# Optimization experiments

Hardware: AMD Instinct MI355X
Metric: run time of the kernel (lower is better)

Reference implementation:

```python
import jax, jax.numpy as jnp
import numpy as np

STRIDE = 1
PADDING = 1
GROUPS = 1


def setup_inputs() -> dict:
    key = jax.random.key(0)
    kx, kw, kb = jax.random.split(key, 3)
    x_int = jax.random.randint(kx, (16, 256, 56, 56), 0, 127, dtype=jnp.int32)
    weight_int = jax.random.randint(kw, (256, 256, 3, 3), 0, 127, dtype=jnp.int32)
    bias_int = jax.random.randint(kb, (256,), 0, 127, dtype=jnp.int32)
    return {"x_int": x_int, "weight_int": weight_int, "bias_int": bias_int}


def reference(x_int, weight_int, bias_int):
    # Integer conv2d with int32 accumulation, exactly F.conv2d semantics.
    y = jax.lax.conv_general_dilated(
        x_int,
        weight_int,
        window_strides=(STRIDE, STRIDE),
        padding=((PADDING, PADDING), (PADDING, PADDING)),
        dimension_numbers=("NCHW", "OIHW", "NCHW"),
        feature_group_count=GROUPS,
    )
    # bias broadcast over [B, Cout, H, W]
    return y + bias_int[None, :, None, None]
```

## Files before the change

### kernel.cpp

```cpp
#include <hip/hip_runtime.h>


typedef int v4i __attribute__((ext_vector_type(4)));

#define X8_ROWSTRIDE 3712
#define X8_IMGSTRIDE (58 * X8_ROWSTRIDE)
#define X8_BYTES (64 * X8_IMGSTRIDE)
#define W8_TILE 36864
#define XS_OFF 36864
#define LDS_BYTES 59648

typedef const __attribute__((address_space(1))) unsigned char* gptr_t;
typedef __attribute__((address_space(3))) unsigned char* lptr_t;

__global__ __launch_bounds__(256)
void pack_all(const int* __restrict__ x, const int* __restrict__ wgt,
              unsigned char* __restrict__ ws8) {
  const int blk = blockIdx.x;
  if (blk < 3712) {
    const int row = blk % 58;
    const int cb  = blk / 58;
    const int chunk = cb >> 4, b = cb & 15;
    const int tid = threadIdx.x;
    if (tid >= 232) return;
    const int slot = tid >> 2, p = tid & 3;
    union { v4i v; unsigned char c[16]; } u;
    u.v = (v4i){0, 0, 0, 0};
    if (row >= 1 && row <= 56 && slot >= 1 && slot <= 56) {
      const int q = (p - (slot >> 2)) & 3;
      const unsigned char* src = (const unsigned char*)(x
          + ((b * 256 + chunk * 64 + q * 16) * 56 + (row - 1)) * 56 + (slot - 1));
      #pragma unroll
      for (int j = 0; j < 16; ++j) u.c[j] = src[j * 12544];
    }
    *(v4i*)(ws8 + cb * X8_IMGSTRIDE + row * X8_ROWSTRIDE + slot * 64 + p * 16) = u.v;
  } else {
    const int g  = (blk - 3712) * 256 + threadIdx.x;
    const int p  = g & 3;
    const int sp = g >> 2;
    const int s  = sp % 9;
    const int ct = sp / 9;
    const int co64 = ct & 63;
    const int tcch = ct >> 6;
    const int tc = tcch >> 2, chunk = tcch & 3;
    const int q = (p - ((co64 >> 2) & 3)) & 3;
    const unsigned char* src = (const unsigned char*)(wgt
        + (tc * 64 + co64) * 2304 + (chunk * 64 + q * 16) * 9 + s);
    union { v4i v; unsigned char c[16]; } u;
    #pragma unroll
    for (int j = 0; j < 16; ++j) u.c[j] = src[j * 36];
    *(v4i*)(ws8 + X8_BYTES + ct * 576 + s * 64 + p * 16) = u.v;
  }
}

__global__ __launch_bounds__(512, 4)
void conv_main(const unsigned char* __restrict__ ws8, const int* __restrict__ bias,
               int* __restrict__ out) {
  __shared__ __align__(16) unsigned char lds[LDS_BYTES];
  unsigned char* wls = lds;
  unsigned char* xs  = lds + XS_OFF;
  const unsigned char* x8 = ws8;
  const unsigned char* w8 = ws8 + X8_BYTES;

  const int tid = threadIdx.x, lane = tid & 63, wv = tid >> 6;
  const int q = lane >> 4, m = lane & 15;
  const int cw = wv & 1;
  const int pw = wv >> 1;
  const int tc = blockIdx.x;
  const int h0 = blockIdx.y * 4;
  const int b  = blockIdx.z;

  const unsigned char* arow = wls + (cw * 32 + m) * 576 + ((q + (m >> 2)) & 3) * 16;
  int boff[3][4];
  #pragma unroll
  for (int kw = 0; kw < 3; ++kw)
    #pragma unroll
    for (int nt = 0; nt < 4; ++nt) {
      int slot = nt * 16 + m + kw;
      slot = slot > 57 ? 57 : slot;
      boff[kw][nt] = slot * 64 + ((q + (slot >> 2)) & 3) * 16;
    }

  v4i acc[2][4];
  #pragma unroll
  for (int i = 0; i < 2; ++i)
    #pragma unroll
    for (int j = 0; j < 4; ++j) acc[i][j] = (v4i){0, 0, 0, 0};

  for (int c = 0; c < 4; ++c) {
    __syncthreads();
    const unsigned char* wg = w8 + (tc * 4 + c) * W8_TILE;
    #pragma unroll
    for (int i = 0; i < 5; ++i) {
      const int j = i * 8 + wv;
      if (j < 36)
        __builtin_amdgcn_global_load_lds((gptr_t)(wg + j * 1024 + lane * 16),
                                         (lptr_t)(wls + j * 1024), 16, 0, 0);
    }
    const unsigned char* xg = x8 + (c * 16 + b) * X8_IMGSTRIDE + h0 * X8_ROWSTRIDE;
    #pragma unroll
    for (int i = 0; i < 3; ++i) {
      const int j = i * 8 + wv;
      if (j < 22)
        __builtin_amdgcn_global_load_lds((gptr_t)(xg + j * 1024 + lane * 16),
                                         (lptr_t)(xs + j * 1024), 16, 0, 0);
    }
    __syncthreads();
    #pragma unroll
    for (int kh = 0; kh < 3; ++kh) {
      const unsigned char* xr = xs + (pw + kh) * X8_ROWSTRIDE;
      #pragma unroll
      for (int kw = 0; kw < 3; ++kw) {
        const int s = kh * 3 + kw;
        const v4i a0 = *(const v4i*)(arow + s * 64);
        const v4i a1 = *(const v4i*)(arow + 16 * 576 + s * 64);
        #pragma unroll
        for (int nt = 0; nt < 4; ++nt) {
          const v4i bf = *(const v4i*)(xr + boff[kw][nt]);
          acc[0][nt] = __builtin_amdgcn_mfma_i32_16x16x64_i8(a0, bf, acc[0][nt], 0, 0, 0);
          acc[1][nt] = __builtin_amdgcn_mfma_i32_16x16x64_i8(a1, bf, acc[1][nt], 0, 0, 0);
        }
      }
    }
  }

  const int h = h0 + pw;
  #pragma unroll
  for (int half = 0; half < 2; ++half) {
    #pragma unroll
    for (int nt = 0; nt < 4; ++nt) {
      const int wp = nt * 16 + m;
      if (wp < 56) {
        #pragma unroll
        for (int r = 0; r < 4; ++r) {
          const int co = tc * 64 + cw * 32 + half * 16 + q * 4 + r;
          out[((b * 256 + co) * 56 + h) * 56 + wp] = acc[half][nt][r] + bias[co];
        }
      }
    }
  }
}

extern "C" void kernel_launch(void* const* d_in, const int* in_sizes, int n_in,
                              void* d_out, int out_size, void* d_ws, size_t ws_size,
                              hipStream_t stream) {
  const int* x    = (const int*)d_in[0];
  const int* w    = (const int*)d_in[1];
  const int* bias = (const int*)d_in[2];
  unsigned char* ws8 = (unsigned char*)d_ws;
  hipLaunchKernelGGL(pack_all, dim3(3712 + 144), dim3(256), 0, stream, x, w, ws8);
  hipLaunchKernelGGL(conv_main, dim3(4, 14, 16), dim3(512), 0, stream,
                     ws8, bias, (int*)d_out);
}
```

Baseline: 136.2 us.

## Switch conv to 32x32x32 int8 MFMA with 32-channel chunks and 128-thread blocks

Result: no change. 135.9 us (-0.2%).

```diff
diff --git a/kernel.cpp b/kernel.cpp
--- a/kernel.cpp
+++ b/kernel.cpp
@@ -1,141 +1,141 @@
 #include <hip/hip_runtime.h>
 
 
-typedef int v4i __attribute__((ext_vector_type(4)));
+typedef int v4i  __attribute__((ext_vector_type(4)));
+typedef int v16i __attribute__((ext_vector_type(16)));
 
-#define X8_ROWSTRIDE 3712
-#define X8_IMGSTRIDE (58 * X8_ROWSTRIDE)
-#define X8_BYTES (64 * X8_IMGSTRIDE)
-#define W8_TILE 36864
-#define XS_OFF 36864
-#define LDS_BYTES 59648
+#define X8_ROWSTRIDE 1856
+#define X8_IMGSTRIDE 107648
+#define X8_BYTES     13778944
+#define W8_CHUNK     18432
 
 typedef const __attribute__((address_space(1))) unsigned char* gptr_t;
 typedef __attribute__((address_space(3))) unsigned char* lptr_t;
 
+__device__ __forceinline__ int pack4(const int* p, int stride) {
+  return (p[0] & 255) | ((p[stride] & 255) << 8) |
+         ((p[2 * stride] & 255) << 16) | ((p[3 * stride] & 255) << 24);
+}
+
 __global__ __launch_bounds__(256)
 void pack_all(const int* __restrict__ x, const int* __restrict__ wgt,
               unsigned char* __restrict__ ws8) {
-  const int blk = blockIdx.x;
-  if (blk < 3712) {
-    const int row = blk % 58;
-    const int cb  = blk / 58;
-    const int chunk = cb >> 4, b = cb & 15;
-    const int tid = threadIdx.x;
-    if (tid >= 232) return;
-    const int slot = tid >> 2, p = tid & 3;
-    union { v4i v; unsigned char c[16]; } u;
-    u.v = (v4i){0, 0, 0, 0};
+  const int g = blockIdx.x * 256 + threadIdx.x;
+  if (g < 861184) {
+    const int p = g & 1;
+    int t = g >> 1;
+    const int slot = t % 58; t /= 58;
+    const int row  = t % 58;
+    const int cb   = t / 58;
+    v4i v = (v4i){0, 0, 0, 0};
     if (row >= 1 && row <= 56 && slot >= 1 && slot <= 56) {
-      const int q = (p - (slot >> 2)) & 3;
-      const unsigned char* src = (const unsigned char*)(x
-          + ((b * 256 + chunk * 64 + q * 16) * 56 + (row - 1)) * 56 + (slot - 1));
-      #pragma unroll
-      for (int j = 0; j < 16; ++j) u.c[j] = src[j * 12544];
+      const int chunk = cb >> 4, b = cb & 15;
+      const int srcg = (p + slot) & 1;
+      const int ci0 = chunk * 32 + srcg * 16;
+      const int* src = x + (b * 256 + ci0) * 3136 + (row - 1) * 56 + (slot - 1);
+      v = (v4i){pack4(src, 3136), pack4(src + 4 * 3136, 3136),
+                pack4(src + 8 * 3136, 3136), pack4(src + 12 * 3136, 3136)};
     }
-    *(v4i*)(ws8 + cb * X8_IMGSTRIDE + row * X8_ROWSTRIDE + slot * 64 + p * 16) = u.v;
+    *(v4i*)(ws8 + (cb * 58 + row) * X8_ROWSTRIDE + slot * 32 + p * 16) = v;
   } else {
-    const int g  = (blk - 3712) * 256 + threadIdx.x;
-    const int p  = g & 3;
-    const int sp = g >> 2;
-    const int s  = sp % 9;
-    const int ct = sp / 9;
-    const int co64 = ct & 63;
-    const int tcch = ct >> 6;
-    const int tc = tcch >> 2, chunk = tcch & 3;
-    const int q = (p - ((co64 >> 2) & 3)) & 3;
-    const unsigned char* src = (const unsigned char*)(wgt
-        + (tc * 64 + co64) * 2304 + (chunk * 64 + q * 16) * 9 + s);
-    union { v4i v; unsigned char c[16]; } u;
-    #pragma unroll
-    for (int j = 0; j < 16; ++j) u.c[j] = src[j * 36];
-    *(v4i*)(ws8 + X8_BYTES + ct * 576 + s * 64 + p * 16) = u.v;
+    const int gw = g - 861184;
+    const int p = gw & 1;
+    int t = gw >> 1;
+    const int tap = t % 9;  t /= 9;
+    const int co = t & 63;
+    const int tcc = t >> 6;
+    const int chunk = tcc & 7, cotile = tcc >> 3;
+    const int srcg = (p + co) & 1;
+    const int ci0 = chunk * 32 + srcg * 16;
+    const int* src = wgt + ((cotile * 64 + co) * 256 + ci0) * 9 + tap;
+    v4i v = (v4i){pack4(src, 9), pack4(src + 36, 9),
+                  pack4(src + 72, 9), pack4(src + 108, 9)};
+    *(v4i*)(ws8 + X8_BYTES + (t * 9 + tap) * 32 + p * 16) = v;
   }
 }
 
-__global__ __launch_bounds__(512, 4)
+__global__ __launch_bounds__(128, 2)
 void conv_main(const unsigned char* __restrict__ ws8, const int* __restrict__ bias,
                int* __restrict__ out) {
-  __shared__ __align__(16) unsigned char lds[LDS_BYTES];
+  __shared__ __align__(16) unsigned char lds[18432 + 12288];
+  __shared__ int bls[64];
   unsigned char* wls = lds;
-  unsigned char* xs  = lds + XS_OFF;
-  const unsigned char* x8 = ws8;
-  const unsigned char* w8 = ws8 + X8_BYTES;
+  unsigned char* xs  = lds + 18432;
 
   const int tid = threadIdx.x, lane = tid & 63, wv = tid >> 6;
-  const int q = lane >> 4, m = lane & 15;
-  const int cw = wv & 1;
-  const int pw = wv >> 1;
+  const int n = lane & 31, gq = lane >> 5;
   const int tc = blockIdx.x;
   const int h0 = blockIdx.y * 4;
   const int b  = blockIdx.z;
 
-  const unsigned char* arow = wls + (cw * 32 + m) * 576 + ((q + (m >> 2)) & 3) * 16;
+  if (tid < 64) bls[tid] = bias[tc * 64 + tid];
+
+  const int abase = n * 288 + (((gq + n) & 1) << 4);
   int boff[3][4];
   #pragma unroll
   for (int kw = 0; kw < 3; ++kw)
     #pragma unroll
-    for (int nt = 0; nt < 4; ++nt) {
-      int slot = nt * 16 + m + kw;
-      slot = slot > 57 ? 57 : slot;
-      boff[kw][nt] = slot * 64 + ((q + (slot >> 2)) & 3) * 16;
+    for (int bt = 0; bt < 4; ++bt) {
+      int slot = bt * 16 + (n & 15) + kw;
+      if (slot > 57) slot = 57;
+      boff[kw][bt] = slot * 32 + (((gq + slot) & 1) << 4);
     }
+  const int rbase = (2 * wv + (n >> 4)) * X8_ROWSTRIDE;
 
-  v4i acc[2][4];
+  v16i acc[2][4];
   #pragma unroll
   for (int i = 0; i < 2; ++i)
     #pragma unroll
-    for (int j = 0; j < 4; ++j) acc[i][j] = (v4i){0, 0, 0, 0};
+    for (int j = 0; j < 4; ++j)
+      acc[i][j] = (v16i){0,0,0,0,0,0,0,0,0,0,0,0,0,0,0,0};
 
-  for (int c = 0; c < 4; ++c) {
+  const unsigned char* wg = ws8 + X8_BYTES + tc * (8 * W8_CHUNK);
+  const unsigned char* xg = ws8 + b * X8_IMGSTRIDE + h0 * X8_ROWSTRIDE;
+
+  for (int c = 0; c < 8; ++c) {
     __syncthreads();
-    const unsigned char* wg = w8 + (tc * 4 + c) * W8_TILE;
+    const gptr_t wsrc = (gptr_t)(wg + c * W8_CHUNK);
     #pragma unroll
-    for (int i = 0; i < 5; ++i) {
-      const int j = i * 8 + wv;
-      if (j < 36)
-        __builtin_amdgcn_global_load_lds((gptr_t)(wg + j * 1024 + lane * 16),
-                                         (lptr_t)(wls + j * 1024), 16, 0, 0);
-    }
-    const unsigned char* xg = x8 + (c * 16 + b) * X8_IMGSTRIDE + h0 * X8_ROWSTRIDE;
+    for (int i = 0; i < 9; ++i)
+      __builtin_amdgcn_global_load_lds(wsrc + i * 2048 + tid * 16,
+                                       (lptr_t)(wls + i * 2048 + tid * 16), 16, 0, 0);
+    const gptr_t xsrc = (gptr_t)(xg + c * (16 * X8_IMGSTRIDE));
     #pragma unroll
-    for (int i = 0; i < 3; ++i) {
-      const int j = i * 8 + wv;
-      if (j < 22)
-        __builtin_amdgcn_global_load_lds((gptr_t)(xg + j * 1024 + lane * 16),
-                                         (lptr_t)(xs + j * 1024), 16, 0, 0);
-    }
+    for (int i = 0; i < 6; ++i)
+      __builtin_amdgcn_global_load_lds(xsrc + i * 2048 + tid * 16,
+                                       (lptr_t)(xs + i * 2048 + tid * 16), 16, 0, 0);
     __syncthreads();
     #pragma unroll
     for (int kh = 0; kh < 3; ++kh) {
-      const unsigned char* xr = xs + (pw + kh) * X8_ROWSTRIDE;
+      const unsigned char* xr = xs + rbase + kh * X8_ROWSTRIDE;
       #pragma unroll
       for (int kw = 0; kw < 3; ++kw) {
-        const int s = kh * 3 + kw;
-        const v4i a0 = *(const v4i*)(arow + s * 64);
-        const v4i a1 = *(const v4i*)(arow + 16 * 576 + s * 64);
+        const int tap = kh * 3 + kw;
+        const v4i a0 = *(const v4i*)(wls + abase + tap * 32);
+        const v4i a1 = *(const v4i*)(wls + 9216 + abase + tap * 32);
         #pragma unroll
-        for (int nt = 0; nt < 4; ++nt) {
-          const v4i bf = *(const v4i*)(xr + boff[kw][nt]);
-          acc[0][nt] = __builtin_amdgcn_mfma_i32_16x16x64_i8(a0, bf, acc[0][nt], 0, 0, 0);
-          acc[1][nt] = __builtin_amdgcn_mfma_i32_16x16x64_i8(a1, bf, acc[1][nt], 0, 0, 0);
+        for (int bt = 0; bt < 4; ++bt) {
+          const v4i bb = *(const v4i*)(xr + boff[kw][bt]);
+          acc[0][bt] = __builtin_amdgcn_mfma_i32_32x32x32_i8(a0, bb, acc[0][bt], 0, 0, 0);
+          acc[1][bt] = __builtin_amdgcn_mfma_i32_32x32x32_i8(a1, bb, acc[1][bt], 0, 0, 0);
         }
       }
     }
   }
 
-  const int h = h0 + pw;
+  const int h = h0 + 2 * wv + (n >> 4);
+  const int wbase = lane & 15;
   #pragma unroll
-  for (int half = 0; half < 2; ++half) {
+  for (int ct = 0; ct < 2; ++ct) {
     #pragma unroll
-    for (int nt = 0; nt < 4; ++nt) {
-      const int wp = nt * 16 + m;
-      if (wp < 56) {
-        #pragma unroll
-        for (int r = 0; r < 4; ++r) {
-          const int co = tc * 64 + cw * 32 + half * 16 + q * 4 + r;
-          out[((b * 256 + co) * 56 + h) * 56 + wp] = acc[half][nt][r] + bias[co];
-        }
+    for (int r = 0; r < 16; ++r) {
+      const int co64 = ct * 32 + (r & 3) + 8 * (r >> 2) + 4 * gq;
+      const int bv = bls[co64];
+      int* orow = out + ((b * 256 + tc * 64 + co64) * 56 + h) * 56;
+      #pragma unroll
+      for (int bt = 0; bt < 4; ++bt) {
+        const int w0 = bt * 16 + wbase;
+        if (w0 < 56) orow[w0] = acc[ct][bt][r] + bv;
       }
     }
   }
@@ -148,7 +148,7 @@
   const int* w    = (const int*)d_in[1];
   const int* bias = (const int*)d_in[2];
   unsigned char* ws8 = (unsigned char*)d_ws;
-  hipLaunchKernelGGL(pack_all, dim3(3712 + 144), dim3(256), 0, stream, x, w, ws8);
-  hipLaunchKernelGGL(conv_main, dim3(4, 14, 16), dim3(512), 0, stream,
+  hipLaunchKernelGGL(pack_all, dim3(3508), dim3(256), 0, stream, x, w, ws8);
+  hipLaunchKernelGGL(conv_main, dim3(4, 14, 16), dim3(128), 0, stream,
                      ws8, bias, (int*)d_out);
 }
```
